# Performance work log

Hardware: AMD Instinct MI355X
Metric: run time of the kernel (lower is better)

The kernel has to match this reference:

```python
import jax, jax.numpy as jnp
import numpy as np

B, C, H, W = 4, 64, 64, 64
C8 = C // 8


def setup_inputs() -> dict:
    key = jax.random.key(0)
    ks = jax.random.split(key, 8)
    s = 1.0 / np.sqrt(C)
    return {
        "x": jax.random.normal(ks[0], (B, C, H, W), dtype=jnp.float32),
        "Wq": jax.random.normal(ks[1], (C8, C), dtype=jnp.float32) * s,
        "bq": jnp.zeros((C8,), dtype=jnp.float32),
        "Wk": jax.random.normal(ks[2], (C8, C), dtype=jnp.float32) * s,
        "bk": jnp.zeros((C8,), dtype=jnp.float32),
        "Wv": jax.random.normal(ks[3], (C, C), dtype=jnp.float32) * s,
        "bv": jnp.zeros((C,), dtype=jnp.float32),
        "gamma": jnp.zeros((1,), dtype=jnp.float32),
    }


def reference(x, Wq, bq, Wk, bk, Wv, bv, gamma):
    b, c, h, w = x.shape
    hw = h * w
    xf = x.reshape(b, c, hw)  # [B, C, HW]
    # 1x1 convs == per-pixel linear projections
    q = jnp.einsum("dc,bcn->bnd", Wq, xf) + bq            # [B, HW, C/8]
    k = jnp.einsum("dc,bcn->bdn", Wk, xf) + bk[:, None]   # [B, C/8, HW]
    v = jnp.einsum("dc,bcn->bdn", Wv, xf) + bv[:, None]   # [B, C, HW]
    scale = 1.0 / jnp.sqrt(jnp.asarray(c // 8, dtype=x.dtype))
    attn = jax.nn.softmax(jnp.einsum("bnd,bdm->bnm", q, k) * scale, axis=-1)  # [B, HW, HW]
    # out[:, :, n] = sum_m attn[n, m] * v[:, :, m]
    out = jnp.einsum("bnm,bcm->bcn", attn, v).reshape(b, c, h, w)
    return gamma[0] * out + x
```

## Files before the change

### kernel.cpp

```cpp
#include <hip/hip_runtime.h>

#define HW 4096

typedef float f32x4 __attribute__((ext_vector_type(4)));
typedef __bf16 bf16x8 __attribute__((ext_vector_type(8)));
typedef short s16x4 __attribute__((ext_vector_type(4)));

union F8 { bf16x8 v; unsigned long long q[2]; unsigned short u[8]; __bf16 h[8]; };

__device__ inline unsigned short f2bf(float f) {
    unsigned int u = __builtin_bit_cast(unsigned int, f);
    u += 0x7fffu + ((u >> 16) & 1u);
    return (unsigned short)(u >> 16);
}
__device__ inline float bf2f(unsigned short h) {
    unsigned int u = ((unsigned int)h) << 16;
    return __builtin_bit_cast(float, u);
}
__device__ inline bf16x8 frag_lo(const unsigned short* p) {
    F8 f; f.q[0] = *(const unsigned long long*)p; f.q[1] = 0ull; return f.v;
}
__device__ inline s16x4 frag4s(const unsigned short* p) {
    union { s16x4 v; unsigned long long q; } f;
    f.q = *(const unsigned long long*)p; return f.v;
}

#define MFMA16(a,b,c) __builtin_amdgcn_mfma_f32_16x16x32_bf16(a, b, c, 0, 0, 0)
#define EXP2(x) __builtin_amdgcn_exp2f(x)

#if defined(__has_builtin)
#if __has_builtin(__builtin_amdgcn_mfma_f32_16x16x16bf16_1k)
#define HAVE_K16 1
__device__ inline f32x4 SMFMA16x16(s16x4 a, s16x4 b, f32x4 c) {
    return __builtin_amdgcn_mfma_f32_16x16x16bf16_1k(a, b, c, 0, 0, 0);
}
#endif
#endif

__global__ __launch_bounds__(256, 4) void proj_kernel(
    const float* __restrict__ x,
    const float* __restrict__ Wq, const float* __restrict__ bq,
    const float* __restrict__ Wk, const float* __restrict__ bk,
    const float* __restrict__ Wv, const float* __restrict__ bv,
    unsigned short* __restrict__ qpack, unsigned short* __restrict__ kpack,
    unsigned short* __restrict__ vt3)
{
    const float A2 = 0.51006977f;
    __shared__ float ldsW[80][64];
    __shared__ float ldsB[80];

    const int blk   = blockIdx.x;
    const int b     = blk >> 8;
    const int rest  = blk & 255;
    const int ntile = rest >> 2;
    const int rg    = rest & 3;
    const int tid   = threadIdx.x;
    const int w     = tid >> 6;
    const int lane  = tid & 63;
    const int n     = ntile * 64 + lane;

#pragma unroll
    for (int kk = 0; kk < 5; ++kk) {
        const int idx = tid + kk * 256;
        const int r   = idx >> 4;
        const int c   = (idx & 15) << 2;
        f32x4 val;
        if (r < 8) { val = *(const f32x4*)(Wq + r * 64 + c); val *= A2; }
        else if (r < 16) val = *(const f32x4*)(Wk + (r - 8) * 64 + c);
        else             val = *(const f32x4*)(Wv + (r - 16) * 64 + c);
        *(f32x4*)(&ldsW[r][c]) = val;
    }
    if (tid < 80) {
        ldsB[tid] = (tid < 8) ? bq[tid] * A2
                  : (tid < 16) ? bk[tid - 8] : bv[tid - 16];
    }
    __syncthreads();

    const float* xb = x + (size_t)b * 64 * HW + n;
    float xv[64];
#pragma unroll
    for (int c = 0; c < 64; ++c) xv[c] = xb[c * HW];

    auto rowdot = [&](int row) -> float {
        const float* wr = &ldsW[row][0];
        float a0 = 0.f, a1 = 0.f, a2 = 0.f, a3 = 0.f;
#pragma unroll
        for (int c4 = 0; c4 < 16; ++c4) {
            f32x4 wv = *(const f32x4*)(wr + c4 * 4);
            a0 = fmaf(wv[0], xv[c4*4+0], a0);
            a1 = fmaf(wv[1], xv[c4*4+1], a1);
            a2 = fmaf(wv[2], xv[c4*4+2], a2);
            a3 = fmaf(wv[3], xv[c4*4+3], a3);
        }
        return (a0 + a1) + (a2 + a3) + ldsB[row];
    };

    const int vslot = (((n >> 2) & 3) << 3) + (n & 3) + (((n >> 4) & 1) << 2);
    unsigned short* vB = vt3 + ((size_t)(b * 128 + (n >> 5)) * 64) * 32 + vslot;

    const int r0 = rg * 20 + w * 5;
#pragma unroll
    for (int rr = 0; rr < 5; ++rr) {
        const int row = r0 + rr;
        float val = rowdot(row);
        if (row < 8) {
            qpack[(size_t)(b * HW + n) * 8 + row] = f2bf(val);
        } else if (row < 16) {
            kpack[(size_t)(b * HW + n) * 8 + (row - 8)] = f2bf(val);
        } else {
            vB[(size_t)(row - 16) * 32] = f2bf(val);
        }
    }
}

__global__ __launch_bounds__(512, 1) void attn_kernel(
    const unsigned short* __restrict__ qpack,
    const unsigned short* __restrict__ kpack,
    const unsigned short* __restrict__ vt3,
    const float* __restrict__ x,
    const float* __restrict__ gamma,
    float* __restrict__ out)
{
    const int blk  = blockIdx.x;
    const int slot = blk & 7;
    const int j32  = blk >> 3;
    const int b    = slot >> 1;
    const int qt   = (j32 << 1) | (slot & 1);
    const int nb   = qt * 64;
    const int tid  = threadIdx.x;
    const int w    = tid >> 6;
    const int lane = tid & 63;
    const int g    = lane >> 4;
    const int ln   = lane & 15;

    __shared__ unsigned short ldsO[4][64][66];
    __shared__ float ldsL[8][64];

#if HAVE_K16
    const s16x4 z4 = {0, 0, 0, 0};
    s16x4 qf[4];
#pragma unroll
    for (int i = 0; i < 4; ++i)
        qf[i] = (g < 2)
              ? frag4s(qpack + (size_t)(b * HW + nb + 16 * i + ln) * 8 + 4 * g)
              : z4;
#else
    F8 zf; zf.q[0] = 0ull; zf.q[1] = 0ull;
    bf16x8 qf[4];
#pragma unroll
    for (int i = 0; i < 4; ++i)
        qf[i] = (g == 0)
              ? frag_lo(qpack + (size_t)(b * HW + nb + 16 * i + ln) * 8)
              : zf.v;
#endif

    f32x4 o[4][4];
    float psum[4];
#pragma unroll
    for (int i = 0; i < 4; ++i) {
#pragma unroll
        for (int j = 0; j < 4; ++j) o[i][j] = (f32x4){0,0,0,0};
        psum[i] = 0.f;
    }

    const int mq = w * 512;
    const unsigned short* kb = kpack + (size_t)(b * HW + mq + ln) * 8;
    const unsigned short* vwin = vt3 + ((size_t)b * 128 + w * 16) * 2048
                               + ln * 32 + 8 * g;

#pragma unroll 2
    for (int ch = 0; ch < 16; ++ch) {
        const unsigned short* kp = kb + ch * 256;
#if HAVE_K16
        s16x4 kf0 = (g < 2) ? frag4s(kp + 4 * g)       : z4;
        s16x4 kf1 = (g < 2) ? frag4s(kp + 128 + 4 * g) : z4;
#else
        bf16x8 kf0 = (g == 0) ? frag_lo(kp)       : zf.v;
        bf16x8 kf1 = (g == 0) ? frag_lo(kp + 128) : zf.v;
#endif
        const unsigned short* vp = vwin + (size_t)ch * 2048;
        bf16x8 vf0 = *(const bf16x8*)(vp);
        bf16x8 vf1 = *(const bf16x8*)(vp + 512);
        bf16x8 vf2 = *(const bf16x8*)(vp + 1024);
        bf16x8 vf3 = *(const bf16x8*)(vp + 1536);

        const f32x4 z = {0.f, 0.f, 0.f, 0.f};
#pragma unroll
        for (int i = 0; i < 4; ++i) {
#if HAVE_K16
            f32x4 s0 = SMFMA16x16(kf0, qf[i], z);
            f32x4 s1 = SMFMA16x16(kf1, qf[i], z);
#else
            f32x4 s0 = MFMA16(kf0, qf[i], z);
            f32x4 s1 = MFMA16(kf1, qf[i], z);
#endif
            F8 pa;
            float sacc = 0.f;
#pragma unroll
            for (int r = 0; r < 4; ++r) {
                float e0 = EXP2(s0[r]);
                float e1 = EXP2(s1[r]);
                sacc += e0 + e1;
                pa.h[r]     = (__bf16)e0;
                pa.h[r + 4] = (__bf16)e1;
            }
            psum[i] += sacc;
            o[i][0] = MFMA16(pa.v, vf0, o[i][0]);
            o[i][1] = MFMA16(pa.v, vf1, o[i][1]);
            o[i][2] = MFMA16(pa.v, vf2, o[i][2]);
            o[i][3] = MFMA16(pa.v, vf3, o[i][3]);
        }
    }

#pragma unroll
    for (int i = 0; i < 4; ++i) {
        psum[i] += __shfl_xor(psum[i], 16);
        psum[i] += __shfl_xor(psum[i], 32);
    }

    if (w < 4) {
#pragma unroll
        for (int i = 0; i < 4; ++i)
#pragma unroll
            for (int r = 0; r < 4; ++r)
#pragma unroll
                for (int j = 0; j < 4; ++j)
                    ldsO[w][16 * i + 4 * g + r][16 * j + ln] = f2bf(o[i][j][r]);
    }
    if (lane < 16) {
#pragma unroll
        for (int i = 0; i < 4; ++i)
            ldsL[w][16 * i + ln] = psum[i];
    }
    __syncthreads();
    if (w >= 4) {
        const int s = w - 4;
#pragma unroll
        for (int i = 0; i < 4; ++i)
#pragma unroll
            for (int r = 0; r < 4; ++r)
#pragma unroll
                for (int j = 0; j < 4; ++j) {
                    unsigned short* p = &ldsO[s][16 * i + 4 * g + r][16 * j + ln];
                    *p = f2bf(bf2f(*p) + o[i][j][r]);
                }
    }
    __syncthreads();

    const int q  = tid & 63;
    const int cg = tid >> 6;
    float L = 0.f;
#pragma unroll
    for (int wv = 0; wv < 8; ++wv) L += ldsL[wv][q];
    const float inv = 1.0f / L;
    const float gm  = gamma[0];
#pragma unroll
    for (int jj = 0; jj < 8; ++jj) {
        const int c = cg + 8 * jj;
        float Ov = bf2f(ldsO[0][q][c]) + bf2f(ldsO[1][q][c])
                 + bf2f(ldsO[2][q][c]) + bf2f(ldsO[3][q][c]);
        const size_t idx = (size_t)(b * 64 + c) * HW + nb + q;
        out[idx] = fmaf(gm, Ov * inv, x[idx]);
    }
}

extern "C" void kernel_launch(void* const* d_in, const int* in_sizes, int n_in,
                              void* d_out, int out_size, void* d_ws, size_t ws_size,
                              hipStream_t stream) {
    const float* x  = (const float*)d_in[0];
    const float* Wq = (const float*)d_in[1];
    const float* bq = (const float*)d_in[2];
    const float* Wk = (const float*)d_in[3];
    const float* bk = (const float*)d_in[4];
    const float* Wv = (const float*)d_in[5];
    const float* bv = (const float*)d_in[6];
    const float* gm = (const float*)d_in[7];

    unsigned short* qpack = (unsigned short*)d_ws;
    unsigned short* kpack = qpack + 4 * HW * 8;
    unsigned short* vt3   = kpack + 4 * HW * 8;
    float* out = (float*)d_out;

    proj_kernel<<<1024, 256, 0, stream>>>(x, Wq, bq, Wk, bk, Wv, bv,
                                          qpack, kpack, vt3);
    attn_kernel<<<256, 512, 0, stream>>>(qpack, kpack, vt3, x, gm, out);
}
```

Measured before the change: 30.82 us.

## Fuse projection and attention kernels with a cooperative grid sync

Merges the projection kernel and the attention kernel into one cooperative launch of 256 blocks of 512 threads. Each block first computes Q/K/V projections for its own 64-pixel tile, all blocks meet at a grid-wide barrier, and then each runs attention on that tile. LDS is shared between the two phases through a union. The aim is to remove the second kernel launch and the gap between kernels. In exchange, the projection phase runs on fewer, wider blocks at occupancy 1, and a grid sync plus the cooperative launch add their own overhead.

```diff
diff --git a/kernel.cpp b/kernel.cpp
--- a/kernel.cpp
+++ b/kernel.cpp
@@ -1,4 +1,7 @@
 #include <hip/hip_runtime.h>
+#include <hip/hip_cooperative_groups.h>
+
+namespace cg = cooperative_groups;
 
 #define HW 4096
 
@@ -37,104 +40,95 @@
 #endif
 #endif
 
-__global__ __launch_bounds__(256, 4) void proj_kernel(
+struct ProjSh { float W[80][64]; float B[80]; };
+struct AttnSh { unsigned short O[4][64][66]; float L[8][64]; };
+
+__global__ __launch_bounds__(512, 1) void fused_kernel(
     const float* __restrict__ x,
     const float* __restrict__ Wq, const float* __restrict__ bq,
     const float* __restrict__ Wk, const float* __restrict__ bk,
     const float* __restrict__ Wv, const float* __restrict__ bv,
     unsigned short* __restrict__ qpack, unsigned short* __restrict__ kpack,
-    unsigned short* __restrict__ vt3)
+    unsigned short* __restrict__ vt3,
+    const float* __restrict__ gamma, float* __restrict__ out)
 {
+    __shared__ __align__(16) char shraw[sizeof(AttnSh)];
+    ProjSh* shp = (ProjSh*)shraw;
+    AttnSh* sha = (AttnSh*)shraw;
+
     const float A2 = 0.51006977f;
-    __shared__ float ldsW[80][64];
-    __shared__ float ldsB[80];
-
-    const int blk   = blockIdx.x;
-    const int b     = blk >> 8;
-    const int rest  = blk & 255;
-    const int ntile = rest >> 2;
-    const int rg    = rest & 3;
-    const int tid   = threadIdx.x;
-    const int w     = tid >> 6;
-    const int lane  = tid & 63;
-    const int n     = ntile * 64 + lane;
-
-#pragma unroll
-    for (int kk = 0; kk < 5; ++kk) {
-        const int idx = tid + kk * 256;
-        const int r   = idx >> 4;
-        const int c   = (idx & 15) << 2;
-        f32x4 val;
-        if (r < 8) { val = *(const f32x4*)(Wq + r * 64 + c); val *= A2; }
-        else if (r < 16) val = *(const f32x4*)(Wk + (r - 8) * 64 + c);
-        else             val = *(const f32x4*)(Wv + (r - 16) * 64 + c);
-        *(f32x4*)(&ldsW[r][c]) = val;
-    }
-    if (tid < 80) {
-        ldsB[tid] = (tid < 8) ? bq[tid] * A2
-                  : (tid < 16) ? bk[tid - 8] : bv[tid - 16];
-    }
-    __syncthreads();
-
-    const float* xb = x + (size_t)b * 64 * HW + n;
-    float xv[64];
-#pragma unroll
-    for (int c = 0; c < 64; ++c) xv[c] = xb[c * HW];
-
-    auto rowdot = [&](int row) -> float {
-        const float* wr = &ldsW[row][0];
-        float a0 = 0.f, a1 = 0.f, a2 = 0.f, a3 = 0.f;
-#pragma unroll
-        for (int c4 = 0; c4 < 16; ++c4) {
-            f32x4 wv = *(const f32x4*)(wr + c4 * 4);
-            a0 = fmaf(wv[0], xv[c4*4+0], a0);
-            a1 = fmaf(wv[1], xv[c4*4+1], a1);
-            a2 = fmaf(wv[2], xv[c4*4+2], a2);
-            a3 = fmaf(wv[3], xv[c4*4+3], a3);
-        }
-        return (a0 + a1) + (a2 + a3) + ldsB[row];
-    };
-
-    const int vslot = (((n >> 2) & 3) << 3) + (n & 3) + (((n >> 4) & 1) << 2);
-    unsigned short* vB = vt3 + ((size_t)(b * 128 + (n >> 5)) * 64) * 32 + vslot;
-
-    const int r0 = rg * 20 + w * 5;
-#pragma unroll
-    for (int rr = 0; rr < 5; ++rr) {
-        const int row = r0 + rr;
-        float val = rowdot(row);
-        if (row < 8) {
-            qpack[(size_t)(b * HW + n) * 8 + row] = f2bf(val);
-        } else if (row < 16) {
-            kpack[(size_t)(b * HW + n) * 8 + (row - 8)] = f2bf(val);
-        } else {
-            vB[(size_t)(row - 16) * 32] = f2bf(val);
-        }
-    }
-}
-
-__global__ __launch_bounds__(512, 1) void attn_kernel(
-    const unsigned short* __restrict__ qpack,
-    const unsigned short* __restrict__ kpack,
-    const unsigned short* __restrict__ vt3,
-    const float* __restrict__ x,
-    const float* __restrict__ gamma,
-    float* __restrict__ out)
-{
     const int blk  = blockIdx.x;
     const int slot = blk & 7;
-    const int j32  = blk >> 3;
     const int b    = slot >> 1;
-    const int qt   = (j32 << 1) | (slot & 1);
-    const int nb   = qt * 64;
+    const int pt   = ((blk >> 3) << 1) | (slot & 1);
     const int tid  = threadIdx.x;
     const int w    = tid >> 6;
     const int lane = tid & 63;
     const int g    = lane >> 4;
     const int ln   = lane & 15;
 
-    __shared__ unsigned short ldsO[4][64][66];
-    __shared__ float ldsL[8][64];
+    {
+        const int n = pt * 64 + lane;
+#pragma unroll
+        for (int kk = 0; kk < 3; ++kk) {
+            const int idx = tid + kk * 512;
+            if (idx < 1280) {
+                const int r = idx >> 4;
+                const int c = (idx & 15) << 2;
+                f32x4 val;
+                if (r < 8) { val = *(const f32x4*)(Wq + r * 64 + c); val *= A2; }
+                else if (r < 16) val = *(const f32x4*)(Wk + (r - 8) * 64 + c);
+                else             val = *(const f32x4*)(Wv + (r - 16) * 64 + c);
+                *(f32x4*)(&shp->W[r][c]) = val;
+            }
+        }
+        if (tid < 80) {
+            shp->B[tid] = (tid < 8) ? bq[tid] * A2
+                        : (tid < 16) ? bk[tid - 8] : bv[tid - 16];
+        }
+        __syncthreads();
+
+        const float* xb = x + (size_t)b * 64 * HW + n;
+        float xv[64];
+#pragma unroll
+        for (int c = 0; c < 64; ++c) xv[c] = xb[c * HW];
+
+        auto rowdot = [&](int row) -> float {
+            const float* wr = &shp->W[row][0];
+            float a0 = 0.f, a1 = 0.f, a2 = 0.f, a3 = 0.f;
+#pragma unroll
+            for (int c4 = 0; c4 < 16; ++c4) {
+                f32x4 wv = *(const f32x4*)(wr + c4 * 4);
+                a0 = fmaf(wv[0], xv[c4*4+0], a0);
+                a1 = fmaf(wv[1], xv[c4*4+1], a1);
+                a2 = fmaf(wv[2], xv[c4*4+2], a2);
+                a3 = fmaf(wv[3], xv[c4*4+3], a3);
+            }
+            return (a0 + a1) + (a2 + a3) + shp->B[row];
+        };
+
+        const int vslot = (((n >> 2) & 3) << 3) + (n & 3) + (((n >> 4) & 1) << 2);
+        unsigned short* vB = vt3 + ((size_t)(b * 128 + (n >> 5)) * 64) * 32 + vslot;
+
+        const int r0 = w * 10;
+#pragma unroll
+        for (int rr = 0; rr < 10; ++rr) {
+            const int row = r0 + rr;
+            float val = rowdot(row);
+            if (row < 8) {
+                qpack[(size_t)(b * HW + n) * 8 + row] = f2bf(val);
+            } else if (row < 16) {
+                kpack[(size_t)(b * HW + n) * 8 + (row - 8)] = f2bf(val);
+            } else {
+                vB[(size_t)(row - 16) * 32] = f2bf(val);
+            }
+        }
+    }
+
+    cg::this_grid().sync();
+
+    const int qt = pt;
+    const int nb = qt * 64;
 
 #if HAVE_K16
     const s16x4 z4 = {0, 0, 0, 0};
@@ -225,12 +219,12 @@
             for (int r = 0; r < 4; ++r)
 #pragma unroll
                 for (int j = 0; j < 4; ++j)
-                    ldsO[w][16 * i + 4 * g + r][16 * j + ln] = f2bf(o[i][j][r]);
+                    sha->O[w][16 * i + 4 * g + r][16 * j + ln] = f2bf(o[i][j][r]);
     }
     if (lane < 16) {
 #pragma unroll
         for (int i = 0; i < 4; ++i)
-            ldsL[w][16 * i + ln] = psum[i];
+            sha->L[w][16 * i + ln] = psum[i];
     }
     __syncthreads();
     if (w >= 4) {
@@ -241,24 +235,24 @@
             for (int r = 0; r < 4; ++r)
 #pragma unroll
                 for (int j = 0; j < 4; ++j) {
-                    unsigned short* p = &ldsO[s][16 * i + 4 * g + r][16 * j + ln];
+                    unsigned short* p = &sha->O[s][16 * i + 4 * g + r][16 * j + ln];
                     *p = f2bf(bf2f(*p) + o[i][j][r]);
                 }
     }
     __syncthreads();
 
     const int q  = tid & 63;
-    const int cg = tid >> 6;
+    const int cg_ = tid >> 6;
     float L = 0.f;
 #pragma unroll
-    for (int wv = 0; wv < 8; ++wv) L += ldsL[wv][q];
+    for (int wv = 0; wv < 8; ++wv) L += sha->L[wv][q];
     const float inv = 1.0f / L;
     const float gm  = gamma[0];
 #pragma unroll
     for (int jj = 0; jj < 8; ++jj) {
-        const int c = cg + 8 * jj;
-        float Ov = bf2f(ldsO[0][q][c]) + bf2f(ldsO[1][q][c])
-                 + bf2f(ldsO[2][q][c]) + bf2f(ldsO[3][q][c]);
+        const int c = cg_ + 8 * jj;
+        float Ov = bf2f(sha->O[0][q][c]) + bf2f(sha->O[1][q][c])
+                 + bf2f(sha->O[2][q][c]) + bf2f(sha->O[3][q][c]);
         const size_t idx = (size_t)(b * 64 + c) * HW + nb + q;
         out[idx] = fmaf(gm, Ov * inv, x[idx]);
     }
@@ -281,7 +275,9 @@
     unsigned short* vt3   = kpack + 4 * HW * 8;
     float* out = (float*)d_out;
 
-    proj_kernel<<<1024, 256, 0, stream>>>(x, Wq, bq, Wk, bk, Wv, bv,
-                                          qpack, kpack, vt3);
-    attn_kernel<<<256, 512, 0, stream>>>(qpack, kpack, vt3, x, gm, out);
-}
+    void* args[] = { (void*)&x, (void*)&Wq, (void*)&bq, (void*)&Wk,
+                     (void*)&bk, (void*)&Wv, (void*)&bv, (void*)&qpack,
+                     (void*)&kpack, (void*)&vt3, (void*)&gm, (void*)&out };
+    hipLaunchCooperativeKernel(fused_kernel, dim3(256), dim3(512),
+                               args, 0, stream);
+}
```

Result: slower. 59.97 us (+94.6%).
